# Kernel tuning notes

Measured on AMD Instinct MI355X. Metric: run time of the kernel, lower is better.

The kernel has to match this reference:

```python
import jax, jax.numpy as jnp
import numpy as np

SIDE = 64; EMB = 16; CH = 64; K = 64; V = 64; L = 8
N = SIDE * SIDE

def _pos_table(side, d):
    pe = np.array([[p / np.power(10000, 2 * (j // 2) / d) for j in range(d)]
                   if p != 0 else np.zeros(d) for p in range(side)])
    pe[1:, 0::2] = np.sin(pe[1:, 0::2])
    pe[1:, 1::2] = np.cos(pe[1:, 1::2])
    return pe.astype(np.float32)  # [side, d]

def _pos_emb():
    # Replicates torch .view(1, emb, side, 1): plain reshape of [side, emb] -> [emb, side]
    t = _pos_table(SIDE, EMB).reshape(EMB, SIDE)
    xe = np.broadcast_to(t[:, :, None], (EMB, SIDE, SIDE))
    ye = np.broadcast_to(t[:, None, :], (EMB, SIDE, SIDE))
    return jnp.asarray(np.concatenate([xe, ye], 0).reshape(1, 2 * EMB, N))

def _conv_mask():
    # CausalConv mask, see_center=False, 5x5: zero center pixel onward in center row, and all rows below
    m = np.ones((CH, 3, 5, 5), np.float32)
    m[:, :, 2, 2:] = 0.0
    m[:, :, 3:, :] = 0.0
    return jnp.asarray(m)

def _lrelu(x):
    return jnp.where(x >= 0, x, 0.01 * x)  # LeakyReLU(0.01)

def _bn(x, g, b, eps=1e-5):
    # training-mode batch norm (biased variance), channel axis = 1
    axes = (0,) + tuple(range(2, x.ndim))
    m = jnp.mean(x, axes, keepdims=True)
    var = jnp.mean((x - m) ** 2, axes, keepdims=True)
    sh = (1, -1) + (1,) * (x.ndim - 2)
    return g.reshape(sh) * (x - m) / jnp.sqrt(var + eps) + b.reshape(sh)

def _cv1(w, b, x):
    # 1x1 Conv1d: [O,I] x [B,I,N] -> [B,O,N]
    return jnp.einsum('oi,bin->bon', w, x) + b[:, None]

def reference(x, conv_w, conv_b, bn0_g, bn0_b, q_w, q_b, fk_w, fk_b, ck_w, ck_b,
              fv_w, fv_b, cv_w, cv_b, bn_g, bn_b, out_w, out_b):
    B = x.shape[0]
    pos = jnp.broadcast_to(_pos_emb(), (B, 2 * EMB, N))
    mask = jnp.tril(jnp.ones((N, N), jnp.float32))

    # masked causal conv input layer + BN + LeakyReLU
    w = conv_w * _conv_mask()
    h = jax.lax.conv_general_dilated(x, w, (1, 1), [(2, 2), (2, 2)],
                                     dimension_numbers=('NCHW', 'OIHW', 'NCHW'))
    h = h + conv_b[None, :, None, None]
    h = _lrelu(_bn(h, bn0_g, bn0_b)).reshape(B, CH, N)

    k0 = jnp.zeros((B, K, N), x.dtype)
    v0 = jnp.zeros((B, V, N), x.dtype)
    inv_sqrt_k = 1.0 / jnp.sqrt(jnp.float32(K))

    def layer(carry, p):
        h, k, v = carry
        qw, qb, fkw, fkb, ckw, ckb, fvw, fvb, cvw, cvb, g, bb = p
        x0 = jnp.concatenate([h, pos], 1)            # [B, CH+32, N]
        x0k = jnp.concatenate([x0, k], 1)            # [B, 160, N]
        x0v = jnp.concatenate([x0, v], 1)
        fk = jax.nn.sigmoid(_cv1(fkw, fkb, x0k))
        ck = _lrelu(_cv1(ckw, ckb, x0k))
        k_new = fk * k + ck                          # highway-gated persistent K
        fv = jax.nn.sigmoid(_cv1(fvw, fvb, x0v))
        cv_ = _lrelu(_cv1(cvw, cvb, x0v))
        v_new = fv * v + cv_
        q = _lrelu(_cv1(qw, qb, x0))                 # [B, K, N]
        attn = jnp.einsum('bkn,bkm->bnm', q, k) * inv_sqrt_k  # uses OLD k
        attn = attn * mask + (1.0 - mask) * (-10000.0)
        attn = jax.nn.softmax(attn, axis=-1) * mask
        out1 = jnp.einsum('bnm,bvm->bvn', attn, v)   # uses OLD v; [B, V, N]
        # original code computes fc(out1) but discards it (out2 overwritten)
        h2 = _lrelu(_bn(out1, g, bb))
        return (h2, k_new, v_new), None

    params = (q_w, q_b, fk_w, fk_b, ck_w, ck_b, fv_w, fv_b, cv_w, cv_b, bn_g, bn_b)
    (h, k, v), _ = jax.lax.scan(layer, (h, k0, v0), params)

    out = jnp.einsum('oi,bin->bon', out_w, h) + out_b[None, :, None]
    return out.reshape(B, out_w.shape[0], SIDE, SIDE)

def setup_inputs() -> dict:
    key = jax.random.key(0)
    ks = jax.random.split(key, 12)
    s = 0.05
    return {
        'x': jax.random.normal(ks[0], (2, 3, 64, 64), jnp.float32),
        'conv_w': jax.random.normal(ks[1], (CH, 3, 5, 5), jnp.float32) * s,
        'conv_b': jnp.zeros((CH,), jnp.float32),
        'bn0_g': jnp.ones((CH,), jnp.float32),
        'bn0_b': jnp.zeros((CH,), jnp.float32),
        'q_w': jax.random.normal(ks[2], (L, K, CH + 2 * EMB), jnp.float32) * s,
        'q_b': jnp.zeros((L, K), jnp.float32),
        'fk_w': jax.random.normal(ks[3], (L, K, CH + K + 2 * EMB), jnp.float32) * s,
        'fk_b': jnp.zeros((L, K), jnp.float32),
        'ck_w': jax.random.normal(ks[4], (L, K, CH + K + 2 * EMB), jnp.float32) * s,
        'ck_b': jnp.zeros((L, K), jnp.float32),
        'fv_w': jax.random.normal(ks[5], (L, V, CH + V + 2 * EMB), jnp.float32) * s,
        'fv_b': jnp.zeros((L, V), jnp.float32),
        'cv_w': jax.random.normal(ks[6], (L, V, CH + V + 2 * EMB), jnp.float32) * s,
        'cv_b': jnp.zeros((L, V), jnp.float32),
        'bn_g': jnp.ones((L, CH), jnp.float32),
        'bn_b': jnp.zeros((L, CH), jnp.float32),
        'out_w': jax.random.normal(ks[7], (100, V), jnp.float32) * s,
        'out_b': jnp.zeros((100,), jnp.float32),
    }
```

## Files before the change

kernel.cpp:

```cpp
#include <hip/hip_runtime.h>

#define NPIX 4096
#define CHN  64

typedef __attribute__((ext_vector_type(8))) short short8;
typedef __attribute__((ext_vector_type(8))) unsigned short ushort8;
typedef __attribute__((ext_vector_type(4))) unsigned short ushort4v;
typedef __attribute__((ext_vector_type(4))) float f32x4;
typedef __attribute__((ext_vector_type(16))) float f32x16;
typedef __attribute__((ext_vector_type(4))) unsigned int uint4v;

__device__ __forceinline__ float lrelu_(float x){ return x >= 0.f ? x : 0.01f*x; }

__device__ __forceinline__ unsigned short f2bf(float x){
  union { float f; unsigned u; } v; v.f = x;
  unsigned r = v.u + 0x7FFF + ((v.u >> 16) & 1);
  return (unsigned short)(r >> 16);
}
__device__ __forceinline__ float bf2f(unsigned short h){
  union { unsigned u; float f; } v; v.u = ((unsigned)h) << 16;
  return v.f;
}
__device__ __forceinline__ float asf_(unsigned u){
  union { unsigned u; float f; } v; v.u = u; return v.f;
}

__global__ void pos_kernel(float* __restrict__ pos){
  int idx = blockIdx.x*256 + threadIdx.x;
  int c = idx >> 12;
  int n = idx & (NPIX-1);
  int bcoord = (c < 16) ? (n >> 6) : (n & 63);
  int a = (c < 16) ? c : (c - 16);
  int flat = a*64 + bcoord;
  int p = flat >> 4;
  int j = flat & 15;
  float val = 0.f;
  if (p != 0){
    float ex = (float)(j & ~1) * (1.f/16.f);
    float w = powf(10000.f, -ex);
    float ang = (float)p * w;
    val = (j & 1) ? cosf(ang) : sinf(ang);
  }
  pos[idx] = val;
}

__global__ void wtr_kernel(const float* __restrict__ qw, const float* __restrict__ fkw,
                           const float* __restrict__ ckw, const float* __restrict__ fvw,
                           const float* __restrict__ cvw, const float* __restrict__ convw,
                           float* __restrict__ wt){
  int idx = blockIdx.x*256 + threadIdx.x;
  if (idx >= 381632) return;
  if (idx < 49152){
    int l = idx / 6144, r = idx % 6144, i = r >> 6, o = r & 63;
    wt[idx] = qw[(l*64 + o)*96 + i];
  } else if (idx < 376832){
    int e = idx - 49152;
    int mat = e / 81920, r = e % 81920;
    int l = r / 10240, rr = r % 10240, i = rr >> 6, o = rr & 63;
    const float* src = (mat==0) ? fkw : (mat==1) ? ckw : (mat==2) ? fvw : cvw;
    wt[idx] = src[(l*64 + o)*160 + i];
  } else {
    int e = idx - 376832;
    int o = e & 63, tap = e >> 6;
    int ci = tap / 25, r = tap % 25;
    wt[idx] = convw[(o*3 + ci)*25 + r];
  }
}

__global__ __launch_bounds__(256) void conv_in_kernel(const float* __restrict__ x,
                                                      const float* __restrict__ cwt,
                                                      const float* __restrict__ cb,
                                                      float* __restrict__ out){
  int t = threadIdx.x;
  int o = t & 63;
  int sub = t >> 6;
  int bid = blockIdx.x;
  int b = bid >> 10;
  int n = ((bid & 1023) << 2) + sub;
  int y = n >> 6, xx = n & 63;
  float acc = cb[o];
  #pragma unroll
  for (int ci=0; ci<3; ++ci){
    const float* xp = x + ((b*3+ci)<<12);
    #pragma unroll
    for (int ky=0; ky<3; ++ky){
      int yy = y + ky - 2;
      if (yy < 0) continue;
      int nk = (ky==2) ? 2 : 5;
      #pragma unroll
      for (int kx=0; kx<5; ++kx){
        if (kx >= nk) break;
        int xc = xx + kx - 2;
        if (xc < 0 || xc > 63) continue;
        acc += xp[(yy<<6) + xc] * cwt[(ci*25 + ky*5 + kx)*64 + o];
      }
    }
  }
  out[(b*CHN+o)*NPIX + n] = acc;
}

__global__ __launch_bounds__(1024) void bn_stats_kernel(const float* __restrict__ xin,
                                                        float* __restrict__ stats){
  int c = blockIdx.x;
  int t = threadIdx.x;
  float s = 0.f, ss = 0.f;
  #pragma unroll
  for (int it=0; it<8; ++it){
    int idx = t + it*1024;
    float v = xin[(((idx>>12))*CHN + c)*NPIX + (idx & (NPIX-1))];
    s += v; ss += v*v;
  }
  #pragma unroll
  for (int o=1; o<64; o<<=1){ s += __shfl_xor(s,o); ss += __shfl_xor(ss,o); }
  __shared__ float ps[16], pq[16];
  if ((t & 63) == 0){ ps[t>>6] = s; pq[t>>6] = ss; }
  __syncthreads();
  if (t == 0){
    float S=0.f, Q=0.f;
    #pragma unroll
    for (int i=0;i<16;++i){ S += ps[i]; Q += pq[i]; }
    float mu = S*(1.f/8192.f);
    float var = Q*(1.f/8192.f) - mu*mu;
    var = fmaxf(var, 0.f);
    stats[c*2]   = mu;
    stats[c*2+1] = rsqrtf(var + 1e-5f);
  }
}

__global__ void bn_apply_kernel(const float* __restrict__ xin, const float* __restrict__ stats,
                                const float* __restrict__ g, const float* __restrict__ bb,
                                float* __restrict__ hout){
  int idx = blockIdx.x*256 + threadIdx.x;
  int e = idx << 2;
  int c = (e >> 12) & 63;
  float mu = stats[c*2], rstd = stats[c*2+1];
  float gain = g[c]*rstd;
  float beta = bb[c] - gain*mu;
  float4 v = *(const float4*)(xin + e);
  float4 r;
  r.x = lrelu_(gain*v.x + beta);
  r.y = lrelu_(gain*v.y + beta);
  r.z = lrelu_(gain*v.z + beta);
  r.w = lrelu_(gain*v.w + beta);
  *(float4*)(hout + e) = r;
}

__global__ __launch_bounds__(256) void bn_apply2_kernel(float* __restrict__ hbuf,
                                                        const float* __restrict__ psum,
                                                        const float* __restrict__ psq,
                                                        const float* __restrict__ g,
                                                        const float* __restrict__ bb){
  int bid = blockIdx.x;
  int ebase = bid << 10;
  int c = (ebase >> 12) & 63;
  int t = threadIdx.x;
  float s = psum[c*256 + t];
  float q = psq[c*256 + t];
  #pragma unroll
  for (int o=1; o<64; o<<=1){ s += __shfl_xor(s,o); q += __shfl_xor(q,o); }
  __shared__ float as[4], aq[4];
  if ((t & 63) == 0){ as[t>>6] = s; aq[t>>6] = q; }
  __syncthreads();
  float S = as[0]+as[1]+as[2]+as[3];
  float Q = aq[0]+aq[1]+aq[2]+aq[3];
  float mu = S*(1.f/8192.f);
  float var = fmaxf(Q*(1.f/8192.f) - mu*mu, 0.f);
  float rstd = rsqrtf(var + 1e-5f);
  float gain = g[c]*rstd;
  float beta = bb[c] - gain*mu;
  float4 v = *(const float4*)(hbuf + ebase + t*4);
  float4 r;
  r.x = lrelu_(gain*v.x + beta);
  r.y = lrelu_(gain*v.y + beta);
  r.z = lrelu_(gain*v.z + beta);
  r.w = lrelu_(gain*v.w + beta);
  *(float4*)(hbuf + ebase + t*4) = r;
}

__global__ __launch_bounds__(256) void cv1_kernel(
    const float* __restrict__ hbuf, const float* __restrict__ pos,
    const float* __restrict__ kold, const float* __restrict__ vold,
    const float* __restrict__ qwt,
    const float* __restrict__ fkwt, const float* __restrict__ ckwt,
    const float* __restrict__ fvwt, const float* __restrict__ cvwt,
    const float* __restrict__ qbi,  const float* __restrict__ fkb,
    const float* __restrict__ ckb,  const float* __restrict__ fvb,
    const float* __restrict__ cvb,
    unsigned short* __restrict__ qh, unsigned short* __restrict__ ql,
    float* __restrict__ knew, unsigned short* __restrict__ khn, unsigned short* __restrict__ kln,
    float* __restrict__ vnew, unsigned short* __restrict__ vhTn, unsigned short* __restrict__ vlTn)
{
  int t = threadIdx.x;
  int o  = t & 63;
  int wv = t >> 6;
  int sec  = blockIdx.x >> 9;
  int bid  = blockIdx.x & 511;
  int b    = bid >> 8;
  int tile = bid & 255;
  int n0 = tile*16 + wv*4;

  const float* hb = hbuf + b*CHN*NPIX + n0;
  const float* pb = pos + n0;

  auto load4 = [&](const float* p, float* dst){
    float4 a = *(const float4*)p;
    dst[0]=a.x; dst[1]=a.y; dst[2]=a.z; dst[3]=a.w;
  };

  float x[4];
  long obase = (long)(b*CHN+o)*NPIX + n0;
  size_t nbase = ((size_t)b*NPIX + n0)*64 + o;

  if (sec == 0){
    float aq[4];
    float bias = qbi[o];
    #pragma unroll
    for (int j=0;j<4;++j) aq[j]=bias;
    #pragma unroll 4
    for (int i=0;i<64;++i){
      load4(hb + i*NPIX, x);
      float w = qwt[i*64 + o];
      #pragma unroll
      for (int j=0;j<4;++j) aq[j] += w*x[j];
    }
    #pragma unroll 4
    for (int i=0;i<32;++i){
      load4(pb + i*NPIX, x);
      float w = qwt[(64+i)*64 + o];
      #pragma unroll
      for (int j=0;j<4;++j) aq[j] += w*x[j];
    }
    const float QS = 0.125f * 1.4426950408889634f;
    #pragma unroll
    for (int j=0;j<4;++j){
      float v = lrelu_(aq[j]) * QS;
      unsigned short hb16 = f2bf(v);
      qh[nbase + (size_t)j*64] = hb16;
      ql[nbase + (size_t)j*64] = f2bf(v - bf2f(hb16));
    }
  } else if (sec == 1){
    const float* kb = kold + b*CHN*NPIX + n0;
    float af[4], ac[4];
    float bf = fkb[o], bc = ckb[o];
    #pragma unroll
    for (int j=0;j<4;++j){ af[j]=bf; ac[j]=bc; }
    #pragma unroll 4
    for (int i=0;i<64;++i){
      load4(hb + i*NPIX, x);
      float wf = fkwt[i*64+o], wc = ckwt[i*64+o];
      #pragma unroll
      for (int j=0;j<4;++j){ af[j] += wf*x[j]; ac[j] += wc*x[j]; }
    }
    #pragma unroll 4
    for (int i=0;i<32;++i){
      load4(pb + i*NPIX, x);
      float wf = fkwt[(64+i)*64+o], wc = ckwt[(64+i)*64+o];
      #pragma unroll
      for (int j=0;j<4;++j){ af[j] += wf*x[j]; ac[j] += wc*x[j]; }
    }
    #pragma unroll 4
    for (int i=0;i<64;++i){
      load4(kb + i*NPIX, x);
      float wf = fkwt[(96+i)*64+o], wc = ckwt[(96+i)*64+o];
      #pragma unroll
      for (int j=0;j<4;++j){ af[j] += wf*x[j]; ac[j] += wc*x[j]; }
    }
    float kv[4];
    load4(kb + o*NPIX, kv);
    #pragma unroll
    for (int j=0;j<4;++j){
      float fk = 1.f/(1.f+__expf(-af[j]));
      float kn = fk*kv[j] + lrelu_(ac[j]);
      knew[obase+j] = kn;
      unsigned short hb16 = f2bf(kn);
      khn[nbase + (size_t)j*64] = hb16;
      kln[nbase + (size_t)j*64] = f2bf(kn - bf2f(hb16));
    }
  } else {
    const float* vb = vold + b*CHN*NPIX + n0;
    float af[4], ac[4];
    float bf = fvb[o], bc = cvb[o];
    #pragma unroll
    for (int j=0;j<4;++j){ af[j]=bf; ac[j]=bc; }
    #pragma unroll 4
    for (int i=0;i<64;++i){
      load4(hb + i*NPIX, x);
      float wf = fvwt[i*64+o], wc = cvwt[i*64+o];
      #pragma unroll
      for (int j=0;j<4;++j){ af[j] += wf*x[j]; ac[j] += wc*x[j]; }
    }
    #pragma unroll 4
    for (int i=0;i<32;++i){
      load4(pb + i*NPIX, x);
      float wf = fvwt[(64+i)*64+o], wc = cvwt[(64+i)*64+o];
      #pragma unroll
      for (int j=0;j<4;++j){ af[j] += wf*x[j]; ac[j] += wc*x[j]; }
    }
    #pragma unroll 4
    for (int i=0;i<64;++i){
      load4(vb + i*NPIX, x);
      float wf = fvwt[(96+i)*64+o], wc = cvwt[(96+i)*64+o];
      #pragma unroll
      for (int j=0;j<4;++j){ af[j] += wf*x[j]; ac[j] += wc*x[j]; }
    }
    float vv[4];
    load4(vb + o*NPIX, vv);
    ushort4v vph, vpl;
    #pragma unroll
    for (int j=0;j<4;++j){
      float fv = 1.f/(1.f+__expf(-af[j]));
      float vn = fv*vv[j] + lrelu_(ac[j]);
      vnew[obase+j] = vn;
      unsigned short hb16 = f2bf(vn);
      vph[j] = hb16;
      vpl[j] = f2bf(vn - bf2f(hb16));
    }
    *(ushort4v*)(vhTn + ((size_t)(b*CHN+o))*NPIX + n0) = vph;
    *(ushort4v*)(vlTn + ((size_t)(b*CHN+o))*NPIX + n0) = vpl;
  }
}

__device__ __forceinline__ void pack_sf(const f32x16& sfv, unsigned (&ph)[4][2],
                                        unsigned (&pl)[4][2]){
  #pragma unroll
  for (int a=0; a<4; ++a){
    unsigned h0, h1;
    asm("v_cvt_pk_bf16_f32 %0, %1, %2" : "=v"(h0) : "v"(sfv[4*a]),   "v"(sfv[4*a+1]));
    asm("v_cvt_pk_bf16_f32 %0, %1, %2" : "=v"(h1) : "v"(sfv[4*a+2]), "v"(sfv[4*a+3]));
    float r0 = sfv[4*a]   - asf_(h0 << 16);
    float r1 = sfv[4*a+1] - asf_(h0 & 0xffff0000u);
    float r2 = sfv[4*a+2] - asf_(h1 << 16);
    float r3 = sfv[4*a+3] - asf_(h1 & 0xffff0000u);
    unsigned l0, l1;
    asm("v_cvt_pk_bf16_f32 %0, %1, %2" : "=v"(l0) : "v"(r0), "v"(r1));
    asm("v_cvt_pk_bf16_f32 %0, %1, %2" : "=v"(l1) : "v"(r2), "v"(r3));
    ph[a][0]=h0; ph[a][1]=h1; pl[a][0]=l0; pl[a][1]=l1;
  }
}

__global__ __launch_bounds__(128) void attn_mfma(
    const unsigned short* __restrict__ qhg, const unsigned short* __restrict__ qlg,
    const unsigned short* __restrict__ khg, const unsigned short* __restrict__ klg,
    const unsigned short* __restrict__ vhg, const unsigned short* __restrict__ vlg,
    float* __restrict__ part)
{
  int bid = 1087 - (int)blockIdx.x;
  int b = 0, id = bid;
  if (id >= 544){ b = 1; id -= 544; }
  int pidx = bid;
  int rem = id, k = 0;
  while (rem >= 4*(k+1)){ rem -= 4*(k+1); ++k; }
  int rt    = 4*k + rem/(k+1);
  int chunk = rem - (rem/(k+1))*(k+1);

  int C0  = chunk << 8;
  int end = min(C0 + 256, rt*64 + 64);
  int nt  = (end - C0 + 63) >> 6;

  int t = threadIdx.x;
  int w = t >> 6;
  int l = t & 63;
  int q = l & 31;
  int hi = l >> 5;
  int qbase = rt*64 + w*32;
  int n_g = qbase + q;
  int nmax_w = qbase + 31;

  __shared__ __align__(16) char KH[8192], KL[8192];
  __shared__ __align__(16) char VH[8192], VL[8192];

  const unsigned short* qhp = qhg + (size_t)b*NPIX*64;
  const unsigned short* qlp = qlg + (size_t)b*NPIX*64;
  const unsigned short* khp = khg + (size_t)b*NPIX*64;
  const unsigned short* klp = klg + (size_t)b*NPIX*64;
  const unsigned short* vhp = vhg + (size_t)b*CHN*NPIX;
  const unsigned short* vlp = vlg + (size_t)b*CHN*NPIX;

  short8 qhf[4], qlf[4];
  #pragma unroll
  for (int kc=0; kc<4; ++kc){
    qhf[kc] = *(const short8*)(qhp + (size_t)n_g*64 + kc*16 + hi*8);
    qlf[kc] = *(const short8*)(qlp + (size_t)n_g*64 + kc*16 + hi*8);
  }

  int srow[4], scc8[4], soff[4];
  #pragma unroll
  for (int p=0; p<4; ++p){
    int slot = t + (p<<7);
    int row = slot >> 3, cc = slot & 7;
    srow[p] = row; scc8[p] = cc*8;
    soff[p] = row*128 + ((cc ^ (row & 7)) << 4);
  }
  ushort8 rkh[4], rkl[4], rvh[4], rvl[4];
  auto issue = [&](int m0){
    #pragma unroll
    for (int p=0; p<4; ++p){
      rkh[p] = *(const ushort8*)(khp + (size_t)(m0+srow[p])*64 + scc8[p]);
      rkl[p] = *(const ushort8*)(klp + (size_t)(m0+srow[p])*64 + scc8[p]);
      rvh[p] = *(const ushort8*)(vhp + (size_t)srow[p]*NPIX + m0 + scc8[p]);
      rvl[p] = *(const ushort8*)(vlp + (size_t)srow[p]*NPIX + m0 + scc8[p]);
    }
  };

  f32x16 oacc0, oacc1;
  #pragma unroll
  for (int i=0; i<16; ++i){ oacc0[i]=0.f; oacc1[i]=0.f; }
  float m_run = -1e30f, l_run = 0.f;

  issue(C0);
  for (int ti=0; ti<nt; ++ti){
    int m0 = C0 + (ti<<6);
    __syncthreads();
    #pragma unroll
    for (int p=0; p<4; ++p){
      *(ushort8*)(KH + soff[p]) = rkh[p];
      *(ushort8*)(KL + soff[p]) = rkl[p];
      *(ushort8*)(VH + soff[p]) = rvh[p];
      *(ushort8*)(VL + soff[p]) = rvl[p];
    }
    __syncthreads();
    if (ti+1 < nt) issue(m0 + 64);

    if (m0 <= nmax_w){
      f32x16 sf0, sf1;
      #pragma unroll
      for (int i=0; i<16; ++i){ sf0[i]=0.f; sf1[i]=0.f; }
      #pragma unroll
      for (int kc=0; kc<4; ++kc){
        int off0 = q*128 + (((2*kc + hi) ^ (q & 7)) << 4);
        short8 ah0 = *(const short8*)(KH + off0);
        short8 al0 = *(const short8*)(KL + off0);
        short8 ah1 = *(const short8*)(KH + off0 + 4096);
        short8 al1 = *(const short8*)(KL + off0 + 4096);
        sf0 = __builtin_amdgcn_mfma_f32_32x32x16_bf16(ah0, qhf[kc], sf0, 0,0,0);
        sf1 = __builtin_amdgcn_mfma_f32_32x32x16_bf16(ah1, qhf[kc], sf1, 0,0,0);
        sf0 = __builtin_amdgcn_mfma_f32_32x32x16_bf16(al0, qhf[kc], sf0, 0,0,0);
        sf1 = __builtin_amdgcn_mfma_f32_32x32x16_bf16(al1, qhf[kc], sf1, 0,0,0);
        sf0 = __builtin_amdgcn_mfma_f32_32x32x16_bf16(ah0, qlf[kc], sf0, 0,0,0);
        sf1 = __builtin_amdgcn_mfma_f32_32x32x16_bf16(ah1, qlf[kc], sf1, 0,0,0);
      }
      float mx = -1e30f;
      #pragma unroll
      for (int r=0; r<16; ++r){
        int mg0 = m0 + (r&3) + 8*(r>>2) + 4*hi;
        float s0 = (mg0 <= n_g) ? sf0[r] : -1e30f;
        float s1 = (mg0 + 32 <= n_g) ? sf1[r] : -1e30f;
        sf0[r] = s0; sf1[r] = s1;
        mx = fmaxf(mx, fmaxf(s0, s1));
      }
      mx = fmaxf(mx, __shfl_xor(mx, 32));
      float m_new = fmaxf(m_run, mx);
      float alpha = exp2f(m_run - m_new);
      float ps = 0.f;
      #pragma unroll
      for (int r=0; r<16; ++r){
        float e0 = exp2f(sf0[r] - m_new);
        float e1 = exp2f(sf1[r] - m_new);
        sf0[r] = e0; sf1[r] = e1;
        ps += e0 + e1;
      }
      ps += __shfl_xor(ps, 32);
      l_run = l_run*alpha + ps;
      m_run = m_new;

      unsigned ph0[4][2], pl0[4][2], ph1[4][2], pl1[4][2];
      pack_sf(sf0, ph0, pl0);
      pack_sf(sf1, ph1, pl1);

      #pragma unroll
      for (int i=0; i<16; ++i){ oacc0[i] *= alpha; oacc1[i] *= alpha; }

#define PV_KC(KC, PH, PL) { \
      const int kk = (KC)&1; \
      unsigned oh0 = hi ? PH[2*kk+1][0] : PH[2*kk][0]; \
      unsigned oh1 = hi ? PH[2*kk+1][1] : PH[2*kk][1]; \
      unsigned sh0 = hi ? PH[2*kk][0]   : PH[2*kk+1][0]; \
      unsigned sh1 = hi ? PH[2*kk][1]   : PH[2*kk+1][1]; \
      unsigned rh0 = __shfl_xor(sh0, 32); \
      unsigned rh1 = __shfl_xor(sh1, 32); \
      unsigned ol0 = hi ? PL[2*kk+1][0] : PL[2*kk][0]; \
      unsigned ol1 = hi ? PL[2*kk+1][1] : PL[2*kk][1]; \
      unsigned sl0 = hi ? PL[2*kk][0]   : PL[2*kk+1][0]; \
      unsigned sl1 = hi ? PL[2*kk][1]   : PL[2*kk+1][1]; \
      unsigned rl0 = __shfl_xor(sl0, 32); \
      unsigned rl1 = __shfl_xor(sl1, 32); \
      union { uint4v u; short8 s; } fh, fl; \
      fh.u[0] = hi ? rh0 : oh0; fh.u[1] = hi ? rh1 : oh1; \
      fh.u[2] = hi ? oh0 : rh0; fh.u[3] = hi ? oh1 : rh1; \
      fl.u[0] = hi ? rl0 : ol0; fl.u[1] = hi ? rl1 : ol1; \
      fl.u[2] = hi ? ol0 : rl0; fl.u[3] = hi ? ol1 : rl1; \
      int poff = q*128 + (((2*(KC) + hi) ^ (q & 7)) << 4); \
      short8 xvh0 = *(const short8*)(VH + poff); \
      short8 xvl0 = *(const short8*)(VL + poff); \
      short8 xvh1 = *(const short8*)(VH + poff + 4096); \
      short8 xvl1 = *(const short8*)(VL + poff + 4096); \
      oacc0 = __builtin_amdgcn_mfma_f32_32x32x16_bf16(xvh0, fh.s, oacc0, 0,0,0); \
      oacc1 = __builtin_amdgcn_mfma_f32_32x32x16_bf16(xvh1, fh.s, oacc1, 0,0,0); \
      oacc0 = __builtin_amdgcn_mfma_f32_32x32x16_bf16(xvl0, fh.s, oacc0, 0,0,0); \
      oacc1 = __builtin_amdgcn_mfma_f32_32x32x16_bf16(xvl1, fh.s, oacc1, 0,0,0); \
      oacc0 = __builtin_amdgcn_mfma_f32_32x32x16_bf16(xvh0, fl.s, oacc0, 0,0,0); \
      oacc1 = __builtin_amdgcn_mfma_f32_32x32x16_bf16(xvh1, fl.s, oacc1, 0,0,0); \
    }
      PV_KC(0, ph0, pl0)
      PV_KC(1, ph0, pl0)
      PV_KC(2, ph1, pl1)
      PV_KC(3, ph1, pl1)
#undef PV_KC
    }
  }

  float* pacc = part + (size_t)pidx * 4224;
  #pragma unroll
  for (int vf=0; vf<2; ++vf){
    #pragma unroll
    for (int qd=0; qd<4; ++qd){
      int vd = 32*vf + 8*qd + 4*hi;
      f32x4 vv;
      vv.x = vf ? oacc1[4*qd]   : oacc0[4*qd];
      vv.y = vf ? oacc1[4*qd+1] : oacc0[4*qd+1];
      vv.z = vf ? oacc1[4*qd+2] : oacc0[4*qd+2];
      vv.w = vf ? oacc1[4*qd+3] : oacc0[4*qd+3];
      *(f32x4*)(pacc + (size_t)(w*32 + q)*64 + vd) = vv;
    }
  }
  if (l < 32){
    pacc[4096 + (w*32 + l)*2]     = m_run;
    pacc[4096 + (w*32 + l)*2 + 1] = l_run;
  }
}

__global__ __launch_bounds__(256) void attn_combine(const float* __restrict__ part,
                                                    float* __restrict__ out1,
                                                    float* __restrict__ psum,
                                                    float* __restrict__ psq){
  int bid = blockIdx.x;
  int b = bid >> 7, rt = bid & 127;
  int rt64 = rt >> 1;
  int g2 = rt64 >> 2;
  int nch = g2 + 1;
  int base = b*544 + 2*g2*(g2+1) + (rt64 & 3)*(g2+1);

  int t = threadIdx.x;
  int nl = t & 31, vq = t >> 5;
  int row64 = (rt & 1)*32 + nl;

  float M = -1e30f;
  #pragma unroll
  for (int c=0; c<16; ++c)
    if (c < nch) M = fmaxf(M, part[(size_t)(base+c)*4224 + 4096 + row64*2]);

  float L = 0.f;
  float val[8];
  #pragma unroll
  for (int jj=0; jj<8; ++jj) val[jj] = 0.f;
  #pragma unroll
  for (int c=0; c<16; ++c){
    if (c < nch){
      const float* pa = part + (size_t)(base+c)*4224;
      float wgt = exp2f(pa[4096 + row64*2] - M);
      L += pa[4096 + row64*2 + 1] * wgt;
      #pragma unroll
      for (int jj=0; jj<8; ++jj) val[jj] += wgt * pa[row64*64 + vq*8 + jj];
    }
  }
  float invL = 1.f / L;
  float s[8], q[8];
  #pragma unroll
  for (int jj=0; jj<8; ++jj){
    float v = val[jj]*invL;
    out1[((size_t)b*CHN + vq*8 + jj)*NPIX + rt*32 + nl] = v;
    s[jj] = v; q[jj] = v*v;
  }
  #pragma unroll
  for (int o2=1; o2<32; o2<<=1){
    #pragma unroll
    for (int jj=0; jj<8; ++jj){
      s[jj] += __shfl_xor(s[jj], o2);
      q[jj] += __shfl_xor(q[jj], o2);
    }
  }
  if (nl == 0){
    #pragma unroll
    for (int jj=0; jj<8; ++jj){
      int c = vq*8 + jj;
      psum[c*256 + bid] = s[jj];
      psq [c*256 + bid] = q[jj];
    }
  }
}

__global__ __launch_bounds__(256) void final_kernel(const float* __restrict__ h,
                                                    const float* __restrict__ ow,
                                                    const float* __restrict__ ob,
                                                    float* __restrict__ out){
  int idx = blockIdx.x*256 + threadIdx.x;
  int b  = idx / 409600;
  int r  = idx - b*409600;
  int oc = r >> 12;
  int n  = r & (NPIX-1);
  const float* hp = h + (size_t)b*CHN*NPIX + n;
  const float* wp = ow + oc*64;
  float acc = ob[oc];
  #pragma unroll
  for (int v=0; v<64; ++v) acc += wp[v]*hp[(size_t)v*NPIX];
  out[idx] = acc;
}

extern "C" void kernel_launch(void* const* d_in, const int* in_sizes, int n_in,
                              void* d_out, int out_size, void* d_ws, size_t ws_size,
                              hipStream_t stream){
  const float* x     = (const float*)d_in[0];
  const float* convw = (const float*)d_in[1];
  const float* convb = (const float*)d_in[2];
  const float* bn0g  = (const float*)d_in[3];
  const float* bn0b  = (const float*)d_in[4];
  const float* qw    = (const float*)d_in[5];
  const float* qbias = (const float*)d_in[6];
  const float* fkw   = (const float*)d_in[7];
  const float* fkb   = (const float*)d_in[8];
  const float* ckw   = (const float*)d_in[9];
  const float* ckb   = (const float*)d_in[10];
  const float* fvw   = (const float*)d_in[11];
  const float* fvb   = (const float*)d_in[12];
  const float* cvw   = (const float*)d_in[13];
  const float* cvb   = (const float*)d_in[14];
  const float* bng   = (const float*)d_in[15];
  const float* bnb   = (const float*)d_in[16];
  const float* ow    = (const float*)d_in[17];
  const float* ob    = (const float*)d_in[18];

  const size_t TEN = (size_t)2*CHN*NPIX;
  const size_t BFU = TEN/2;
  float* ws   = (float*)d_ws;
  float* pos  = ws;
  float* h    = pos + 32*NPIX;
  float* k0   = h  + TEN;
  float* k1   = k0 + TEN;
  float* v0   = k1 + TEN;
  float* v1   = v0 + TEN;
  float* stats = v1 + TEN;
  float* psum = stats + 128;
  float* psq  = psum + 64*256;
  float* wt   = psq + 64*256;
  float* bfb  = wt + 381632;
  unsigned short* qh  = (unsigned short*)(bfb);
  unsigned short* ql  = (unsigned short*)(bfb + BFU);
  unsigned short* kh0 = (unsigned short*)(bfb + 2*BFU);
  unsigned short* kh1 = (unsigned short*)(bfb + 3*BFU);
  unsigned short* kl0 = (unsigned short*)(bfb + 4*BFU);
  unsigned short* kl1 = (unsigned short*)(bfb + 5*BFU);
  unsigned short* vh0 = (unsigned short*)(bfb + 6*BFU);
  unsigned short* vh1 = (unsigned short*)(bfb + 7*BFU);
  unsigned short* vl0 = (unsigned short*)(bfb + 8*BFU);
  unsigned short* vl1 = (unsigned short*)(bfb + 9*BFU);
  float* part = bfb + 10*BFU;

  hipMemsetAsync(k0, 0, TEN*sizeof(float), stream);
  hipMemsetAsync(v0, 0, TEN*sizeof(float), stream);
  hipMemsetAsync(kh0, 0, TEN*2, stream);
  hipMemsetAsync(kl0, 0, TEN*2, stream);
  hipMemsetAsync(vh0, 0, TEN*2, stream);
  hipMemsetAsync(vl0, 0, TEN*2, stream);

  pos_kernel<<<512,256,0,stream>>>(pos);
  wtr_kernel<<<1491,256,0,stream>>>(qw, fkw, ckw, fvw, cvw, convw, wt);
  conv_in_kernel<<<2048,256,0,stream>>>(x, wt + 376832, convb, h);
  bn_stats_kernel<<<64,1024,0,stream>>>(h, stats);
  bn_apply_kernel<<<512,256,0,stream>>>(h, stats, bn0g, bn0b, h);

  float* kfp[2] = {k0,k1};
  float* vfp[2] = {v0,v1};
  unsigned short* khb[2] = {kh0,kh1};
  unsigned short* klb[2] = {kl0,kl1};
  unsigned short* vhb[2] = {vh0,vh1};
  unsigned short* vlb[2] = {vl0,vl1};
  for (int l=0; l<8; ++l){
    float* kold = kfp[l&1]; float* knew = kfp[(l+1)&1];
    float* vold = vfp[l&1]; float* vnew = vfp[(l+1)&1];
    cv1_kernel<<<1536,256,0,stream>>>(h, pos, kold, vold,
        wt + l*6144,
        wt + 49152 + l*10240,
        wt + 49152 + 81920 + l*10240,
        wt + 49152 + 2*81920 + l*10240,
        wt + 49152 + 3*81920 + l*10240,
        qbias + l*64, fkb + l*64, ckb + l*64, fvb + l*64, cvb + l*64,
        qh, ql,
        knew, khb[(l+1)&1], klb[(l+1)&1],
        vnew, vhb[(l+1)&1], vlb[(l+1)&1]);
    attn_mfma<<<1088,128,0,stream>>>(qh, ql, khb[l&1], klb[l&1], vhb[l&1], vlb[l&1], part);
    attn_combine<<<256,256,0,stream>>>(part, h, psum, psq);
    bn_apply2_kernel<<<512,256,0,stream>>>(h, psum, psq, bng + l*64, bnb + l*64);
  }
  final_kernel<<<3200,256,0,stream>>>(h, ow, ob, (float*)d_out);
}
```

Baseline: 854.9 us.

## Shrink attention blocks to single-wave 32-row tiles with 32-key steps

Restructures the causal attention kernel so each block is one 64-lane wave handling 32 query rows and walking 32-key tiles instead of 64. This doubles the grid, removes the __syncthreads barriers and the per-wave skip of fully masked tiles, and adds s_setprio around the MFMA sequences. V is staged in a new padded, swizzled shared layout, and the combine kernel's indexing is updated for the new partial-result layout. The trade-off is less K/V reuse per staged tile, more partial records to combine, and more per-tile softmax overhead relative to MFMA work.

```diff
diff --git a/kernel.cpp b/kernel.cpp
--- a/kernel.cpp
+++ b/kernel.cpp
@@ -338,36 +338,32 @@
   }
 }
 
-__global__ __launch_bounds__(128) void attn_mfma(
+__global__ __launch_bounds__(64) void attn_mfma(
     const unsigned short* __restrict__ qhg, const unsigned short* __restrict__ qlg,
     const unsigned short* __restrict__ khg, const unsigned short* __restrict__ klg,
     const unsigned short* __restrict__ vhg, const unsigned short* __restrict__ vlg,
     float* __restrict__ part)
 {
-  int bid = 1087 - (int)blockIdx.x;
+  int bid = 2175 - (int)blockIdx.x;
   int b = 0, id = bid;
-  if (id >= 544){ b = 1; id -= 544; }
+  if (id >= 1088){ b = 1; id -= 1088; }
   int pidx = bid;
   int rem = id, k = 0;
-  while (rem >= 4*(k+1)){ rem -= 4*(k+1); ++k; }
-  int rt    = 4*k + rem/(k+1);
+  while (rem >= 8*(k+1)){ rem -= 8*(k+1); ++k; }
+  int rt    = 8*k + rem/(k+1);
   int chunk = rem - (rem/(k+1))*(k+1);
 
   int C0  = chunk << 8;
-  int end = min(C0 + 256, rt*64 + 64);
-  int nt  = (end - C0 + 63) >> 6;
-
-  int t = threadIdx.x;
-  int w = t >> 6;
-  int l = t & 63;
+  int end = min(C0 + 256, rt*32 + 32);
+  int nt  = (end - C0 + 31) >> 5;
+
+  int l = threadIdx.x;
   int q = l & 31;
   int hi = l >> 5;
-  int qbase = rt*64 + w*32;
-  int n_g = qbase + q;
-  int nmax_w = qbase + 31;
-
-  __shared__ __align__(16) char KH[8192], KL[8192];
-  __shared__ __align__(16) char VH[8192], VL[8192];
+  int n_g = rt*32 + q;
+
+  __shared__ __align__(16) char KH[4096], KL[4096];
+  __shared__ __align__(16) char VH[5120], VL[5120];
 
   const unsigned short* qhp = qhg + (size_t)b*NPIX*64;
   const unsigned short* qlp = qlg + (size_t)b*NPIX*64;
@@ -383,22 +379,25 @@
     qlf[kc] = *(const short8*)(qlp + (size_t)n_g*64 + kc*16 + hi*8);
   }
 
-  int srow[4], scc8[4], soff[4];
+  int kRow[4], kCc8[4], kOff[4], vRow[4], vCc8[4], vOff[4];
   #pragma unroll
   for (int p=0; p<4; ++p){
-    int slot = t + (p<<7);
-    int row = slot >> 3, cc = slot & 7;
-    srow[p] = row; scc8[p] = cc*8;
-    soff[p] = row*128 + ((cc ^ (row & 7)) << 4);
+    int slot = l + (p<<6);
+    int kr = slot >> 3, kc = slot & 7;
+    kRow[p] = kr; kCc8[p] = kc*8;
+    kOff[p] = kr*128 + ((kc ^ (kr & 7)) << 4);
+    int vr = slot >> 2, vc = slot & 3;
+    vRow[p] = vr; vCc8[p] = vc*8;
+    vOff[p] = vr*80 + ((vc ^ (vr & 3)) << 4);
   }
   ushort8 rkh[4], rkl[4], rvh[4], rvl[4];
   auto issue = [&](int m0){
     #pragma unroll
     for (int p=0; p<4; ++p){
-      rkh[p] = *(const ushort8*)(khp + (size_t)(m0+srow[p])*64 + scc8[p]);
-      rkl[p] = *(const ushort8*)(klp + (size_t)(m0+srow[p])*64 + scc8[p]);
-      rvh[p] = *(const ushort8*)(vhp + (size_t)srow[p]*NPIX + m0 + scc8[p]);
-      rvl[p] = *(const ushort8*)(vlp + (size_t)srow[p]*NPIX + m0 + scc8[p]);
+      rkh[p] = *(const ushort8*)(khp + (size_t)(m0+kRow[p])*64 + kCc8[p]);
+      rkl[p] = *(const ushort8*)(klp + (size_t)(m0+kRow[p])*64 + kCc8[p]);
+      rvh[p] = *(const ushort8*)(vhp + (size_t)vRow[p]*NPIX + m0 + vCc8[p]);
+      rvl[p] = *(const ushort8*)(vlp + (size_t)vRow[p]*NPIX + m0 + vCc8[p]);
     }
   };
 
@@ -409,107 +408,99 @@
 
   issue(C0);
   for (int ti=0; ti<nt; ++ti){
-    int m0 = C0 + (ti<<6);
-    __syncthreads();
+    int m0 = C0 + (ti<<5);
     #pragma unroll
     for (int p=0; p<4; ++p){
-      *(ushort8*)(KH + soff[p]) = rkh[p];
-      *(ushort8*)(KL + soff[p]) = rkl[p];
-      *(ushort8*)(VH + soff[p]) = rvh[p];
-      *(ushort8*)(VL + soff[p]) = rvl[p];
-    }
-    __syncthreads();
-    if (ti+1 < nt) issue(m0 + 64);
-
-    if (m0 <= nmax_w){
-      f32x16 sf0, sf1;
-      #pragma unroll
-      for (int i=0; i<16; ++i){ sf0[i]=0.f; sf1[i]=0.f; }
-      #pragma unroll
-      for (int kc=0; kc<4; ++kc){
-        int off0 = q*128 + (((2*kc + hi) ^ (q & 7)) << 4);
-        short8 ah0 = *(const short8*)(KH + off0);
-        short8 al0 = *(const short8*)(KL + off0);
-        short8 ah1 = *(const short8*)(KH + off0 + 4096);
-        short8 al1 = *(const short8*)(KL + off0 + 4096);
-        sf0 = __builtin_amdgcn_mfma_f32_32x32x16_bf16(ah0, qhf[kc], sf0, 0,0,0);
-        sf1 = __builtin_amdgcn_mfma_f32_32x32x16_bf16(ah1, qhf[kc], sf1, 0,0,0);
-        sf0 = __builtin_amdgcn_mfma_f32_32x32x16_bf16(al0, qhf[kc], sf0, 0,0,0);
-        sf1 = __builtin_amdgcn_mfma_f32_32x32x16_bf16(al1, qhf[kc], sf1, 0,0,0);
-        sf0 = __builtin_amdgcn_mfma_f32_32x32x16_bf16(ah0, qlf[kc], sf0, 0,0,0);
-        sf1 = __builtin_amdgcn_mfma_f32_32x32x16_bf16(ah1, qlf[kc], sf1, 0,0,0);
-      }
-      float mx = -1e30f;
-      #pragma unroll
-      for (int r=0; r<16; ++r){
-        int mg0 = m0 + (r&3) + 8*(r>>2) + 4*hi;
-        float s0 = (mg0 <= n_g) ? sf0[r] : -1e30f;
-        float s1 = (mg0 + 32 <= n_g) ? sf1[r] : -1e30f;
-        sf0[r] = s0; sf1[r] = s1;
-        mx = fmaxf(mx, fmaxf(s0, s1));
-      }
-      mx = fmaxf(mx, __shfl_xor(mx, 32));
-      float m_new = fmaxf(m_run, mx);
-      float alpha = exp2f(m_run - m_new);
-      float ps = 0.f;
-      #pragma unroll
-      for (int r=0; r<16; ++r){
-        float e0 = exp2f(sf0[r] - m_new);
-        float e1 = exp2f(sf1[r] - m_new);
-        sf0[r] = e0; sf1[r] = e1;
-        ps += e0 + e1;
-      }
-      ps += __shfl_xor(ps, 32);
-      l_run = l_run*alpha + ps;
-      m_run = m_new;
-
-      unsigned ph0[4][2], pl0[4][2], ph1[4][2], pl1[4][2];
-      pack_sf(sf0, ph0, pl0);
-      pack_sf(sf1, ph1, pl1);
-
-      #pragma unroll
-      for (int i=0; i<16; ++i){ oacc0[i] *= alpha; oacc1[i] *= alpha; }
-
-#define PV_KC(KC, PH, PL) { \
-      const int kk = (KC)&1; \
-      unsigned oh0 = hi ? PH[2*kk+1][0] : PH[2*kk][0]; \
-      unsigned oh1 = hi ? PH[2*kk+1][1] : PH[2*kk][1]; \
-      unsigned sh0 = hi ? PH[2*kk][0]   : PH[2*kk+1][0]; \
-      unsigned sh1 = hi ? PH[2*kk][1]   : PH[2*kk+1][1]; \
-      unsigned rh0 = __shfl_xor(sh0, 32); \
-      unsigned rh1 = __shfl_xor(sh1, 32); \
-      unsigned ol0 = hi ? PL[2*kk+1][0] : PL[2*kk][0]; \
-      unsigned ol1 = hi ? PL[2*kk+1][1] : PL[2*kk][1]; \
-      unsigned sl0 = hi ? PL[2*kk][0]   : PL[2*kk+1][0]; \
-      unsigned sl1 = hi ? PL[2*kk][1]   : PL[2*kk+1][1]; \
-      unsigned rl0 = __shfl_xor(sl0, 32); \
-      unsigned rl1 = __shfl_xor(sl1, 32); \
-      union { uint4v u; short8 s; } fh, fl; \
-      fh.u[0] = hi ? rh0 : oh0; fh.u[1] = hi ? rh1 : oh1; \
-      fh.u[2] = hi ? oh0 : rh0; fh.u[3] = hi ? oh1 : rh1; \
-      fl.u[0] = hi ? rl0 : ol0; fl.u[1] = hi ? rl1 : ol1; \
-      fl.u[2] = hi ? ol0 : rl0; fl.u[3] = hi ? ol1 : rl1; \
-      int poff = q*128 + (((2*(KC) + hi) ^ (q & 7)) << 4); \
-      short8 xvh0 = *(const short8*)(VH + poff); \
-      short8 xvl0 = *(const short8*)(VL + poff); \
-      short8 xvh1 = *(const short8*)(VH + poff + 4096); \
-      short8 xvl1 = *(const short8*)(VL + poff + 4096); \
-      oacc0 = __builtin_amdgcn_mfma_f32_32x32x16_bf16(xvh0, fh.s, oacc0, 0,0,0); \
-      oacc1 = __builtin_amdgcn_mfma_f32_32x32x16_bf16(xvh1, fh.s, oacc1, 0,0,0); \
-      oacc0 = __builtin_amdgcn_mfma_f32_32x32x16_bf16(xvl0, fh.s, oacc0, 0,0,0); \
-      oacc1 = __builtin_amdgcn_mfma_f32_32x32x16_bf16(xvl1, fh.s, oacc1, 0,0,0); \
-      oacc0 = __builtin_amdgcn_mfma_f32_32x32x16_bf16(xvh0, fl.s, oacc0, 0,0,0); \
-      oacc1 = __builtin_amdgcn_mfma_f32_32x32x16_bf16(xvh1, fl.s, oacc1, 0,0,0); \
-    }
-      PV_KC(0, ph0, pl0)
-      PV_KC(1, ph0, pl0)
-      PV_KC(2, ph1, pl1)
-      PV_KC(3, ph1, pl1)
+      *(ushort8*)(KH + kOff[p]) = rkh[p];
+      *(ushort8*)(KL + kOff[p]) = rkl[p];
+      *(ushort8*)(VH + vOff[p]) = rvh[p];
+      *(ushort8*)(VL + vOff[p]) = rvl[p];
+    }
+    if (ti+1 < nt) issue(m0 + 32);
+
+    f32x16 sf0;
+    #pragma unroll
+    for (int i=0; i<16; ++i) sf0[i]=0.f;
+    __builtin_amdgcn_s_setprio(1);
+    #pragma unroll
+    for (int kc=0; kc<4; ++kc){
+      int off0 = q*128 + (((2*kc + hi) ^ (q & 7)) << 4);
+      short8 ah0 = *(const short8*)(KH + off0);
+      short8 al0 = *(const short8*)(KL + off0);
+      sf0 = __builtin_amdgcn_mfma_f32_32x32x16_bf16(ah0, qhf[kc], sf0, 0,0,0);
+      sf0 = __builtin_amdgcn_mfma_f32_32x32x16_bf16(al0, qhf[kc], sf0, 0,0,0);
+      sf0 = __builtin_amdgcn_mfma_f32_32x32x16_bf16(ah0, qlf[kc], sf0, 0,0,0);
+    }
+    __builtin_amdgcn_s_setprio(0);
+
+    float mx = -1e30f;
+    #pragma unroll
+    for (int r=0; r<16; ++r){
+      int mg0 = m0 + (r&3) + 8*(r>>2) + 4*hi;
+      float s0 = (mg0 <= n_g) ? sf0[r] : -1e30f;
+      sf0[r] = s0;
+      mx = fmaxf(mx, s0);
+    }
+    mx = fmaxf(mx, __shfl_xor(mx, 32));
+    float m_new = fmaxf(m_run, mx);
+    float alpha = exp2f(m_run - m_new);
+    float ps = 0.f;
+    #pragma unroll
+    for (int r=0; r<16; ++r){
+      float e0 = exp2f(sf0[r] - m_new);
+      sf0[r] = e0;
+      ps += e0;
+    }
+    ps += __shfl_xor(ps, 32);
+    l_run = l_run*alpha + ps;
+    m_run = m_new;
+
+    unsigned ph0[4][2], pl0[4][2];
+    pack_sf(sf0, ph0, pl0);
+
+    #pragma unroll
+    for (int i=0; i<16; ++i){ oacc0[i] *= alpha; oacc1[i] *= alpha; }
+
+#define PV_KC(KC) { \
+    const int kk = (KC); \
+    unsigned oh0 = hi ? ph0[2*kk+1][0] : ph0[2*kk][0]; \
+    unsigned oh1 = hi ? ph0[2*kk+1][1] : ph0[2*kk][1]; \
+    unsigned sh0 = hi ? ph0[2*kk][0]   : ph0[2*kk+1][0]; \
+    unsigned sh1 = hi ? ph0[2*kk][1]   : ph0[2*kk+1][1]; \
+    unsigned rh0 = __shfl_xor(sh0, 32); \
+    unsigned rh1 = __shfl_xor(sh1, 32); \
+    unsigned ol0 = hi ? pl0[2*kk+1][0] : pl0[2*kk][0]; \
+    unsigned ol1 = hi ? pl0[2*kk+1][1] : pl0[2*kk][1]; \
+    unsigned sl0 = hi ? pl0[2*kk][0]   : pl0[2*kk+1][0]; \
+    unsigned sl1 = hi ? pl0[2*kk][1]   : pl0[2*kk+1][1]; \
+    unsigned rl0 = __shfl_xor(sl0, 32); \
+    unsigned rl1 = __shfl_xor(sl1, 32); \
+    union { uint4v u; short8 s; } fh, fl; \
+    fh.u[0] = hi ? rh0 : oh0; fh.u[1] = hi ? rh1 : oh1; \
+    fh.u[2] = hi ? oh0 : rh0; fh.u[3] = hi ? oh1 : rh1; \
+    fl.u[0] = hi ? rl0 : ol0; fl.u[1] = hi ? rl1 : ol1; \
+    fl.u[2] = hi ? ol0 : rl0; fl.u[3] = hi ? ol1 : rl1; \
+    int vch = ((2*kk + hi) ^ (q & 3)) << 4; \
+    short8 xvh0 = *(const short8*)(VH + q*80 + vch); \
+    short8 xvl0 = *(const short8*)(VL + q*80 + vch); \
+    int vch1 = ((2*kk + hi) ^ (q & 3)) << 4; \
+    short8 xvh1 = *(const short8*)(VH + 2560 + q*80 + vch1); \
+    short8 xvl1 = *(const short8*)(VL + 2560 + q*80 + vch1); \
+    __builtin_amdgcn_s_setprio(1); \
+    oacc0 = __builtin_amdgcn_mfma_f32_32x32x16_bf16(xvh0, fh.s, oacc0, 0,0,0); \
+    oacc1 = __builtin_amdgcn_mfma_f32_32x32x16_bf16(xvh1, fh.s, oacc1, 0,0,0); \
+    oacc0 = __builtin_amdgcn_mfma_f32_32x32x16_bf16(xvl0, fh.s, oacc0, 0,0,0); \
+    oacc1 = __builtin_amdgcn_mfma_f32_32x32x16_bf16(xvl1, fh.s, oacc1, 0,0,0); \
+    oacc0 = __builtin_amdgcn_mfma_f32_32x32x16_bf16(xvh0, fl.s, oacc0, 0,0,0); \
+    oacc1 = __builtin_amdgcn_mfma_f32_32x32x16_bf16(xvh1, fl.s, oacc1, 0,0,0); \
+    __builtin_amdgcn_s_setprio(0); \
+  }
+    PV_KC(0)
+    PV_KC(1)
 #undef PV_KC
-    }
-  }
-
-  float* pacc = part + (size_t)pidx * 4224;
+  }
+
+  float* pacc = part + (size_t)pidx * 2112;
   #pragma unroll
   for (int vf=0; vf<2; ++vf){
     #pragma unroll
@@ -520,12 +511,12 @@
       vv.y = vf ? oacc1[4*qd+1] : oacc0[4*qd+1];
       vv.z = vf ? oacc1[4*qd+2] : oacc0[4*qd+2];
       vv.w = vf ? oacc1[4*qd+3] : oacc0[4*qd+3];
-      *(f32x4*)(pacc + (size_t)(w*32 + q)*64 + vd) = vv;
-    }
-  }
-  if (l < 32){
-    pacc[4096 + (w*32 + l)*2]     = m_run;
-    pacc[4096 + (w*32 + l)*2 + 1] = l_run;
+      *(f32x4*)(pacc + (size_t)q*64 + vd) = vv;
+    }
+  }
+  if (hi == 0){
+    pacc[2048 + q*2]     = m_run;
+    pacc[2048 + q*2 + 1] = l_run;
   }
 }
 
@@ -535,19 +526,17 @@
                                                     float* __restrict__ psq){
   int bid = blockIdx.x;
   int b = bid >> 7, rt = bid & 127;
-  int rt64 = rt >> 1;
-  int g2 = rt64 >> 2;
-  int nch = g2 + 1;
-  int base = b*544 + 2*g2*(g2+1) + (rt64 & 3)*(g2+1);
+  int g = rt >> 3;
+  int nch = g + 1;
+  int base = b*1088 + 4*g*(g+1) + (rt & 7)*(g+1);
 
   int t = threadIdx.x;
   int nl = t & 31, vq = t >> 5;
-  int row64 = (rt & 1)*32 + nl;
 
   float M = -1e30f;
   #pragma unroll
   for (int c=0; c<16; ++c)
-    if (c < nch) M = fmaxf(M, part[(size_t)(base+c)*4224 + 4096 + row64*2]);
+    if (c < nch) M = fmaxf(M, part[(size_t)(base+c)*2112 + 2048 + nl*2]);
 
   float L = 0.f;
   float val[8];
@@ -556,11 +545,11 @@
   #pragma unroll
   for (int c=0; c<16; ++c){
     if (c < nch){
-      const float* pa = part + (size_t)(base+c)*4224;
-      float wgt = exp2f(pa[4096 + row64*2] - M);
-      L += pa[4096 + row64*2 + 1] * wgt;
-      #pragma unroll
-      for (int jj=0; jj<8; ++jj) val[jj] += wgt * pa[row64*64 + vq*8 + jj];
+      const float* pa = part + (size_t)(base+c)*2112;
+      float wgt = exp2f(pa[2048 + nl*2] - M);
+      L += pa[2048 + nl*2 + 1] * wgt;
+      #pragma unroll
+      for (int jj=0; jj<8; ++jj) val[jj] += wgt * pa[nl*64 + vq*8 + jj];
     }
   }
   float invL = 1.f / L;
@@ -687,7 +676,7 @@
         qh, ql,
         knew, khb[(l+1)&1], klb[(l+1)&1],
         vnew, vhb[(l+1)&1], vlb[(l+1)&1]);
-    attn_mfma<<<1088,128,0,stream>>>(qh, ql, khb[l&1], klb[l&1], vhb[l&1], vlb[l&1], part);
+    attn_mfma<<<2176,64,0,stream>>>(qh, ql, khb[l&1], klb[l&1], vhb[l&1], vlb[l&1], part);
     attn_combine<<<256,256,0,stream>>>(part, h, psum, psq);
     bn_apply2_kernel<<<512,256,0,stream>>>(h, psum, psq, bng + l*64, bnb + l*64);
   }
```

New measurement: 886.6 us. +3.7%, slower.
